# Optimization experiments

Hardware: AMD Instinct MI355X
Metric: run time of the kernel (lower is better)

The kernel has to match this reference:

```python
import jax, jax.numpy as jnp
import numpy as np

H = 512
B = 32
T = 2048


def setup_inputs() -> dict:
    key = jax.random.key(0)
    ks = jax.random.split(key, 8)
    hidden = jax.random.normal(ks[0], (1, B, H), dtype=jnp.float32)
    encoder_outputs = jax.random.normal(ks[1], (T, B, H), dtype=jnp.float32)
    coverage = jax.random.uniform(ks[2], (B, T), dtype=jnp.float32)
    # nn.Linear(3H, H): weight [H, 3H], bias [H]
    W_attn = jax.random.normal(ks[3], (H, 3 * H), dtype=jnp.float32) / np.sqrt(3 * H)
    b_attn = jax.random.normal(ks[4], (H,), dtype=jnp.float32) / np.sqrt(3 * H)
    # v ~ Normal(0, 1/sqrt(H))
    v = jax.random.normal(ks[5], (H,), dtype=jnp.float32) / np.sqrt(H)
    # nn.Linear(1, H, bias=False): weight [H, 1]
    W_cov = jax.random.normal(ks[6], (H, 1), dtype=jnp.float32)
    return {"hidden": hidden, "encoder_outputs": encoder_outputs, "coverage": coverage,
            "W_attn": W_attn, "b_attn": b_attn, "v": v, "W_cov": W_cov}


def reference(hidden, encoder_outputs, coverage, W_attn, b_attn, v, W_cov):
    # hidden: [1,B,H], encoder_outputs: [T,B,H], coverage: [B,T]
    enc = jnp.transpose(encoder_outputs, (1, 0, 2))          # [B,T,H]
    b, t, h = enc.shape
    hrep = jnp.broadcast_to(hidden[0][:, None, :], (b, t, h))  # [B,T,H]
    # coverage_feature = Linear(1,H,bias=False)(coverage[...,None]) -> outer product
    cov_feat = coverage[..., None] * W_cov[:, 0]               # [B,T,H]
    x = jnp.concatenate([hrep, enc, cov_feat], axis=-1)        # [B,T,3H]
    energy = jax.nn.relu(jnp.einsum('btk,hk->bth', x, W_attn) + b_attn)  # [B,T,H]
    scores = jnp.einsum('bth,h->bt', energy, v)                # [B,T]
    attn_weights = jax.nn.softmax(scores, axis=1)              # softmax over T
    coverage_new = coverage + attn_weights                     # [B,T]
    return attn_weights[:, None, :], coverage_new
```

## Files before the change

### kernel.cpp

```cpp
#include <hip/hip_runtime.h>
#include <hip/hip_bf16.h>

typedef unsigned short u16;
typedef unsigned int u32;
typedef __attribute__((ext_vector_type(8))) short bf16x8;
typedef __attribute__((ext_vector_type(4))) float f32x4;

#define T_DIM 2048
#define B_DIM 32
#define H_DIM 512
#define M_DIM (T_DIM * B_DIM)

__device__ inline unsigned pack2(float a, float b) {
  union { __hip_bfloat162 h2; unsigned u; } c;
  c.h2 = __float22bfloat162_rn(make_float2(a, b));
  return c.u;
}

__device__ __forceinline__ void gld16(const void* g, void* s) {
  __builtin_amdgcn_global_load_lds(
      (const __attribute__((address_space(1))) void*)g,
      (__attribute__((address_space(3))) void*)s, 16, 0, 0);
}

__global__ __launch_bounds__(256) void prep_kernel(
    const float* __restrict__ hidden, const float* __restrict__ W_attn,
    const float* __restrict__ b_attn, const float* __restrict__ W_cov,
    u16* __restrict__ W2bf, float* __restrict__ r, float* __restrict__ u)
{
  const int tid = blockIdx.x * 256 + threadIdx.x;
  const int pair = tid >> 2;
  const int kq = tid & 3;
  const int b = pair >> 9, h = pair & 511;

  {
    const float* hid = hidden + b * 512 + kq * 128;
    const float* w1 = W_attn + (size_t)h * 1536 + kq * 128;
    float acc = 0.f;
    #pragma unroll 8
    for (int k = 0; k < 128; k += 4) {
      float4 x = *(const float4*)(hid + k);
      float4 w = *(const float4*)(w1 + k);
      acc += x.x * w.x + x.y * w.y + x.z * w.z + x.w * w.w;
    }
    acc += __shfl_xor(acc, 1);
    acc += __shfl_xor(acc, 2);
    if (kq == 0) r[pair] = acc + b_attn[h];
  }

  {
    int j0 = tid * 4;
    int hh = j0 >> 9, kk = j0 & 511;
    float4 w = *(const float4*)(W_attn + (size_t)hh * 1536 + 512 + kk);
    uint2 p;
    p.x = pack2(w.x, w.y);
    p.y = pack2(w.z, w.w);
    int f = hh >> 4, c = hh & 15;
    int ks = kk >> 5, quad = (kk >> 3) & 3, e = kk & 7;
    *(uint2*)(W2bf + (size_t)((f * 16 + ks) * 64 + quad * 16 + c) * 8 + e) = p;
  }

  if (tid < 2048) {
    int h3 = tid >> 2;
    const float* w3 = W_attn + (size_t)h3 * 1536 + 1024 + kq * 128;
    const float* wc = W_cov + kq * 128;
    float su = 0.f;
    #pragma unroll 8
    for (int k = 0; k < 128; k += 4) {
      float4 a = *(const float4*)(w3 + k);
      float4 c = *(const float4*)(wc + k);
      su += a.x * c.x + a.y * c.y + a.z * c.z + a.w * c.w;
    }
    su += __shfl_xor(su, 1);
    su += __shfl_xor(su, 2);
    if (kq == 0) u[h3] = su;
  }
}

__global__ __launch_bounds__(512, 4) void gemm_score(
    const float* __restrict__ enc, const u16* __restrict__ W2bf,
    const float* __restrict__ r, const float* __restrict__ u,
    const float* __restrict__ vv, const float* __restrict__ cov,
    float* __restrict__ part)
{
  const int t = blockIdx.x;
  const int m0 = t * 32;
  const int tid = threadIdx.x;
  const int lane = tid & 63;
  const int w = tid >> 6;
  const int quad = lane >> 4, col = lane & 15;

  __shared__ float As[32 * 512];

  #pragma unroll
  for (int q = 0; q < 8; ++q) {
    int n = w * 8 + q;
    int rr = n >> 1, hh = n & 1;
    int gsrc = hh * 64 + (lane ^ (rr & 7));
    gld16(enc + (size_t)(m0 + rr) * 512 + gsrc * 4, (void*)(As + n * 256));
  }
  __syncthreads();

  f32x4 acc[2][4] = {};
  const u16* bbase = W2bf + (size_t)w * 32768 + lane * 8;

  bf16x8 bcur[4], bnxt[4];
  #pragma unroll
  for (int j = 0; j < 4; ++j)
    bcur[j] = *(const bf16x8*)(bbase + j * 8192);

  const int o0 = (((quad * 2)    ) ^ (col & 7)) * 4;
  const int o1 = (((quad * 2) + 1) ^ (col & 7)) * 4;
  const float* arow0 = As + col * 512;

  #pragma unroll
  for (int ks = 0; ks < 16; ++ks) {
    if (ks < 15) {
      #pragma unroll
      for (int j = 0; j < 4; ++j)
        bnxt[j] = *(const bf16x8*)(bbase + j * 8192 + (ks + 1) * 512);
    }
    #pragma unroll
    for (int i = 0; i < 2; ++i) {
      const float* ap = arow0 + i * 8192 + ks * 32;
      float4 f0 = *(const float4*)(ap + o0);
      float4 f1 = *(const float4*)(ap + o1);
      union { bf16x8 v; u32 uu[4]; } af;
      af.uu[0] = pack2(f0.x, f0.y);
      af.uu[1] = pack2(f0.z, f0.w);
      af.uu[2] = pack2(f1.x, f1.y);
      af.uu[3] = pack2(f1.z, f1.w);
      #pragma unroll
      for (int j = 0; j < 4; ++j)
        acc[i][j] = __builtin_amdgcn_mfma_f32_16x16x32_bf16(af.v, bcur[j], acc[i][j], 0, 0, 0);
    }
    #pragma unroll
    for (int j = 0; j < 4; ++j) bcur[j] = bnxt[j];
  }

  float uj[4], vj[4];
  #pragma unroll
  for (int j = 0; j < 4; ++j) {
    int gh = w * 64 + j * 16 + col;
    uj[j] = u[gh];
    vj[j] = vv[gh];
  }
  #pragma unroll
  for (int i = 0; i < 2; ++i) {
    #pragma unroll
    for (int reg = 0; reg < 4; ++reg) {
      int b = i * 16 + quad * 4 + reg;
      float cv = cov[b * 2048 + t];
      float s = 0.f;
      #pragma unroll
      for (int j = 0; j < 4; ++j) {
        float rv = r[b * 512 + w * 64 + j * 16 + col];
        float e = acc[i][j][reg] + rv + cv * uj[j];
        e = fmaxf(e, 0.f);
        s += e * vj[j];
      }
      s += __shfl_xor(s, 1);
      s += __shfl_xor(s, 2);
      s += __shfl_xor(s, 4);
      s += __shfl_xor(s, 8);
      if (col == 0) part[(size_t)(w * 32 + b) * 2048 + t] = s;
    }
  }
}

__global__ __launch_bounds__(256) void softmax_kernel(
    const float* __restrict__ part, const float* __restrict__ cov, float* __restrict__ out)
{
  const int b = blockIdx.x;
  const int tid = threadIdx.x;
  const int lane = tid & 63, wid = tid >> 6;
  __shared__ float red[4];
  float loc[8];
  float lmax = -3.4e38f;
  #pragma unroll
  for (int i = 0; i < 8; ++i) {
    int t = tid + i * 256;
    float s = 0.f;
    #pragma unroll
    for (int p = 0; p < 8; ++p) s += part[(size_t)(p * 32 + b) * 2048 + t];
    loc[i] = s;
    lmax = fmaxf(lmax, s);
  }
  #pragma unroll
  for (int o = 32; o; o >>= 1) lmax = fmaxf(lmax, __shfl_xor(lmax, o));
  if (lane == 0) red[wid] = lmax;
  __syncthreads();
  float bmax = fmaxf(fmaxf(red[0], red[1]), fmaxf(red[2], red[3]));
  __syncthreads();
  float lsum = 0.f;
  #pragma unroll
  for (int i = 0; i < 8; ++i) { loc[i] = __expf(loc[i] - bmax); lsum += loc[i]; }
  #pragma unroll
  for (int o = 32; o; o >>= 1) lsum += __shfl_xor(lsum, o);
  if (lane == 0) red[wid] = lsum;
  __syncthreads();
  float inv = 1.0f / (red[0] + red[1] + red[2] + red[3]);
  #pragma unroll
  for (int i = 0; i < 8; ++i) {
    int t = tid + i * 256;
    float a = loc[i] * inv;
    out[b * 2048 + t] = a;
    out[65536 + b * 2048 + t] = cov[b * 2048 + t] + a;
  }
}

extern "C" void kernel_launch(void* const* d_in, const int* in_sizes, int n_in,
                              void* d_out, int out_size, void* d_ws, size_t ws_size,
                              hipStream_t stream) {
  const float* hidden = (const float*)d_in[0];
  const float* enc    = (const float*)d_in[1];
  const float* cov    = (const float*)d_in[2];
  const float* W_attn = (const float*)d_in[3];
  const float* b_attn = (const float*)d_in[4];
  const float* vv     = (const float*)d_in[5];
  const float* W_cov  = (const float*)d_in[6];
  float* out = (float*)d_out;

  u16* W2bf = (u16*)d_ws;
  float* r  = (float*)((char*)d_ws + 512 * 1024);
  float* u  = r + 32 * 512;
  float* part = u + 512;

  hipLaunchKernelGGL(prep_kernel, dim3(256), dim3(256), 0, stream,
                     hidden, W_attn, b_attn, W_cov, W2bf, r, u);
  hipLaunchKernelGGL(gemm_score, dim3(2048), dim3(512), 0, stream,
                     enc, W2bf, r, u, vv, cov, part);
  hipLaunchKernelGGL(softmax_kernel, dim3(32), dim3(256), 0, stream,
                     part, cov, out);
}
```

Baseline: 280.6 us.

## Double-buffer A/B operands, reduce warp partials in-block, remap block order

Swaps the GEMM main loop's single-step B prefetch for a two-deep register double buffer, and also prefetches the LDS A fragments one k-step ahead. The eight per-warp partial scores are now summed through shared memory inside each block, so the softmax kernel reads one value per (b,t) instead of eight. Block indices are permuted so consecutive blocks touch strided t values, which changes the L2 and channel access pattern. This costs more registers and an extra block barrier in exchange for better load latency hiding and less global traffic.

```diff
diff --git a/kernel.cpp b/kernel.cpp
--- a/kernel.cpp
+++ b/kernel.cpp
@@ -83,7 +83,8 @@
     const float* __restrict__ vv, const float* __restrict__ cov,
     float* __restrict__ part)
 {
-  const int t = blockIdx.x;
+  const int bid = blockIdx.x;
+  const int t = (bid & 7) * 256 + (bid >> 3);
   const int m0 = t * 32;
   const int tid = threadIdx.x;
   const int lane = tid & 63;
@@ -104,27 +105,39 @@
   f32x4 acc[2][4] = {};
   const u16* bbase = W2bf + (size_t)w * 32768 + lane * 8;
 
-  bf16x8 bcur[4], bnxt[4];
-  #pragma unroll
-  for (int j = 0; j < 4; ++j)
-    bcur[j] = *(const bf16x8*)(bbase + j * 8192);
+  bf16x8 bb[2][4];
+  #pragma unroll
+  for (int j = 0; j < 4; ++j) {
+    bb[0][j] = *(const bf16x8*)(bbase + j * 8192);
+    bb[1][j] = *(const bf16x8*)(bbase + j * 8192 + 512);
+  }
 
   const int o0 = (((quad * 2)    ) ^ (col & 7)) * 4;
   const int o1 = (((quad * 2) + 1) ^ (col & 7)) * 4;
   const float* arow0 = As + col * 512;
 
+  float4 areg[2][2][2];
+  #pragma unroll
+  for (int i = 0; i < 2; ++i) {
+    const float* ap = arow0 + i * 8192;
+    areg[0][i][0] = *(const float4*)(ap + o0);
+    areg[0][i][1] = *(const float4*)(ap + o1);
+  }
+
   #pragma unroll
   for (int ks = 0; ks < 16; ++ks) {
     if (ks < 15) {
       #pragma unroll
-      for (int j = 0; j < 4; ++j)
-        bnxt[j] = *(const bf16x8*)(bbase + j * 8192 + (ks + 1) * 512);
+      for (int i = 0; i < 2; ++i) {
+        const float* ap = arow0 + i * 8192 + (ks + 1) * 32;
+        areg[(ks + 1) & 1][i][0] = *(const float4*)(ap + o0);
+        areg[(ks + 1) & 1][i][1] = *(const float4*)(ap + o1);
+      }
     }
     #pragma unroll
     for (int i = 0; i < 2; ++i) {
-      const float* ap = arow0 + i * 8192 + ks * 32;
-      float4 f0 = *(const float4*)(ap + o0);
-      float4 f1 = *(const float4*)(ap + o1);
+      float4 f0 = areg[ks & 1][i][0];
+      float4 f1 = areg[ks & 1][i][1];
       union { bf16x8 v; u32 uu[4]; } af;
       af.uu[0] = pack2(f0.x, f0.y);
       af.uu[1] = pack2(f0.z, f0.w);
@@ -132,10 +145,13 @@
       af.uu[3] = pack2(f1.z, f1.w);
       #pragma unroll
       for (int j = 0; j < 4; ++j)
-        acc[i][j] = __builtin_amdgcn_mfma_f32_16x16x32_bf16(af.v, bcur[j], acc[i][j], 0, 0, 0);
-    }
-    #pragma unroll
-    for (int j = 0; j < 4; ++j) bcur[j] = bnxt[j];
+        acc[i][j] = __builtin_amdgcn_mfma_f32_16x16x32_bf16(af.v, bb[ks & 1][j], acc[i][j], 0, 0, 0);
+    }
+    if (ks < 14) {
+      #pragma unroll
+      for (int j = 0; j < 4; ++j)
+        bb[ks & 1][j] = *(const bf16x8*)(bbase + j * 8192 + (ks + 2) * 512);
+    }
   }
 
   float uj[4], vj[4];
@@ -145,6 +161,10 @@
     uj[j] = u[gh];
     vj[j] = vv[gh];
   }
+
+  __syncthreads();
+  float* red = As;
+
   #pragma unroll
   for (int i = 0; i < 2; ++i) {
     #pragma unroll
@@ -163,8 +183,15 @@
       s += __shfl_xor(s, 2);
       s += __shfl_xor(s, 4);
       s += __shfl_xor(s, 8);
-      if (col == 0) part[(size_t)(w * 32 + b) * 2048 + t] = s;
-    }
+      if (col == 0) red[w * 32 + b] = s;
+    }
+  }
+  __syncthreads();
+  if (tid < 32) {
+    float s = 0.f;
+    #pragma unroll
+    for (int p = 0; p < 8; ++p) s += red[p * 32 + tid];
+    part[(size_t)tid * 2048 + t] = s;
   }
 }
 
@@ -180,9 +207,7 @@
   #pragma unroll
   for (int i = 0; i < 8; ++i) {
     int t = tid + i * 256;
-    float s = 0.f;
-    #pragma unroll
-    for (int p = 0; p < 8; ++p) s += part[(size_t)(p * 32 + b) * 2048 + t];
+    float s = part[(size_t)b * 2048 + t];
     loc[i] = s;
     lmax = fmaxf(lmax, s);
   }
```

Result: faster. 267.4 us (-4.7%).
